# Performance work log

Hardware: AMD Instinct MI355X
Metric: run time of the kernel (lower is better)

## Reference

```python
import jax, jax.numpy as jnp
import numpy as np
from jax import lax

B, L, E, R = 128, 8, 384, 500
HP, HM, HD = 4, 6, 2   # pair-encoder heads, final-mha heads, dynamic-memory heads
MAXLEN = 8
EPS = 1e-5


def _ln(x, g, b):
    m = x.mean(-1, keepdims=True)
    v = ((x - m) ** 2).mean(-1, keepdims=True)
    return (x - m) / jnp.sqrt(v + EPS) * g + b


def _gelu(x):
    return jax.nn.gelu(x, approximate=False)


def _mha(qi, ki, vi, in_w, in_b, out_w, out_b, h):
    # torch nn.MultiheadAttention with packed in_proj ([3E,E]) and out_proj
    Em = qi.shape[-1]
    dh = Em // h
    q = qi @ in_w[:Em].T + in_b[:Em]
    k = ki @ in_w[Em:2 * Em].T + in_b[Em:2 * Em]
    v = vi @ in_w[2 * Em:].T + in_b[2 * Em:]
    def sp(x):
        b_, l_, _ = x.shape
        return x.reshape(b_, l_, h, dh).transpose(0, 2, 1, 3)
    q, k, v = sp(q), sp(k), sp(v)
    a = jax.nn.softmax(jnp.einsum('bhqd,bhkd->bhqk', q, k) / jnp.sqrt(jnp.float32(dh)), axis=-1)
    o = jnp.einsum('bhqk,bhkd->bhqd', a, v).transpose(0, 2, 1, 3).reshape(qi.shape)
    return o @ out_w.T + out_b


def _forward(inputs, emb, rel_pos, qkv_dyn_w, qkv_dyn_b, out_dyn_w, out_dyn_b,
             ln_dyn_g, ln_dyn_b, conv_w, conv_b, tl_in_w, tl_in_b, tl_out_w, tl_out_b,
             tl_ln1_g, tl_ln1_b, tl_ln2_g, tl_ln2_b, tl_ff1_w, tl_ff1_b, tl_ff2_w, tl_ff2_b,
             fc_score_w, fc_score_b, fcq_w, fcq_b, fck_w, fck_b, fcv_w, fcv_b,
             mha_in_w, mha_in_b, mha_out_w, mha_out_b, lnf1_g, lnf1_b, lnf2_g, lnf2_b,
             ff1_w, ff1_b, ff2_w, ff2_b):
    # ---- update_memory: 2-head self-attention over relation embeddings ----
    rel_emb = emb[:R]                                   # [R,E]
    qkv = rel_emb @ qkv_dyn_w.T + qkv_dyn_b             # [R,3E]
    qm, km, vm = jnp.split(qkv, 3, axis=-1)
    dh = E // HD
    def sph(x):
        return x.reshape(R, HD, dh).transpose(1, 0, 2)  # [HD,R,dh]
    qm, km, vm = sph(qm), sph(km), sph(vm)
    am = jax.nn.softmax(jnp.einsum('hqd,hkd->hqk', qm, km) / jnp.sqrt(jnp.float32(dh)), axis=-1)
    om = jnp.einsum('hqk,hkd->hqd', am, vm).transpose(1, 0, 2).reshape(R, E)
    om = om @ out_dyn_w.T + out_dyn_b
    relation_mem = _ln(rel_emb + om, ln_dyn_g, ln_dyn_b)  # [R,E]

    def pair_encode(x):  # x: [N,2,E]  Conv1d(k=3,pad=1) + 2 post-norm transformer layers
        xc = lax.conv_general_dilated(x.transpose(0, 2, 1), conv_w, (1,), [(1, 1)],
                                      dimension_numbers=('NCH', 'OIH', 'NCH'))
        x = (xc + conv_b[None, :, None]).transpose(0, 2, 1)
        for l in range(2):
            a = _mha(x, x, x, tl_in_w[l], tl_in_b[l], tl_out_w[l], tl_out_b[l], HP)
            x = _ln(x + a, tl_ln1_g[l], tl_ln1_b[l])
            f = _gelu(x @ tl_ff1_w[l].T + tl_ff1_b[l]) @ tl_ff2_w[l].T + tl_ff2_b[l]
            x = _ln(x + f, tl_ln2_g[l], tl_ln2_b[l])
        return x

    def fuse(pair):  # pair: [B,1,E] -> memory_attention_fuse
        mem = jnp.concatenate([jnp.broadcast_to(relation_mem[None], (B, R, E)), pair], axis=1)
        q = pair @ fcq_w.T + fcq_b
        k = mem @ fck_w.T + fck_b
        v = mem @ fcv_w.T + fcv_b
        a = _mha(q, k, v, mha_in_w, mha_in_b, mha_out_w, mha_out_b, HM)
        x = _ln(pair + a, lnf1_g, lnf1_b)
        f = _gelu(x @ ff1_w.T + ff1_b) @ ff2_w.T + ff2_b
        return _ln(x + f, lnf2_g, lnf2_b)

    pos = jnp.minimum(jnp.arange(L), MAXLEN - 1)
    seq = emb[inputs] + rel_pos[pos]                    # [B,L,E]

    losses = []
    for _ in range(L - 1):                              # L-1 sequential reduce steps
        Lc = seq.shape[1]
        if Lc <= 2:
            losses.append(jnp.zeros((B, 1), jnp.float32))
            continue
        # all adjacent pairs at once (replaces the per-pair python loop)
        pairs = jnp.stack([seq[:, :-1], seq[:, 1:]], axis=2) + rel_pos[:2]  # [B,Lc-1,2,E]
        hid = pair_encode(pairs.reshape(B * (Lc - 1), 2, E))[:, -1, :].reshape(B, Lc - 1, E)
        sc = jax.nn.sigmoid(hid @ fc_score_w.T + fc_score_b)[..., 0]        # [B,Lc-1]
        idx = jnp.argmax(sc, axis=-1)                                       # [B]
        logp = jax.nn.log_softmax(sc, axis=-1)
        losses.append(-(jnp.exp(logp) * logp).sum(-1, keepdims=True))       # entropy [B,1]
        sel = jnp.take_along_axis(hid, idx[:, None, None], axis=1)          # [B,1,E]
        fused = fuse(sel)                                                   # [B,1,E]
        # scatter fused at idx, delete row idx+1 (compaction)
        updated = jnp.where(jnp.arange(Lc)[None, :, None] == idx[:, None, None], fused, seq)
        gidx = jnp.arange(Lc - 1)[None, :]
        gidx = gidx + (gidx >= (idx + 1)[:, None])
        seq = jnp.take_along_axis(updated, gidx[:, :, None], axis=1)        # [B,Lc-1,E]

    # ---- final memory_attention ----
    Lf = seq.shape[1]  # == 2
    mem = jnp.concatenate([jnp.broadcast_to(relation_mem[None], (B, R, E)), seq], axis=1)
    q = seq @ fcq_w.T + fcq_b
    k = mem @ fck_w.T + fck_b
    a = _mha(q, k, k, mha_in_w, mha_in_b, mha_out_w, mha_out_b, HM)
    x = _ln(seq + a, lnf1_g, lnf1_b)
    f = _gelu(x @ ff1_w.T + ff1_b) @ ff2_w.T + ff2_b
    x = _ln(x + f, lnf2_g, lnf2_b)
    logits = jnp.einsum('ble,bme->blm', x, mem) / jnp.sqrt(jnp.float32(E))
    gate = jnp.ones((R + Lf,), jnp.float32)             # gate_mask buffer is all ones
    logits = logits * gate                              # [B,Lf,R+Lf]
    logp2 = jax.nn.log_softmax(logits, axis=-1)
    ent = -(jnp.exp(logp2) * logp2).sum(-1)             # [B,Lf]
    loss = jnp.concatenate(losses + [ent], axis=-1)     # [B,L+1]
    pred = logits[:, -1, :]                             # [B,R+Lf]
    return pred, loss


def setup_inputs():
    key = jax.random.key(0)
    ctr = [0]
    def nk():
        ctr[0] += 1
        return jax.random.fold_in(key, ctr[0])
    def W(*s):
        return jax.random.normal(nk(), s, jnp.float32) * 0.02
    def Z(*s):
        return jnp.zeros(s, jnp.float32)
    def O(*s):
        return jnp.ones(s, jnp.float32)
    d = {}
    d['inputs'] = jax.random.randint(nk(), (B, L), 0, R)
    d['emb'] = W(R + 1, E).at[R].set(0.0)  # padding_idx row zero
    d['rel_pos'] = W(MAXLEN, E)
    d['qkv_dyn_w'] = W(3 * E, E); d['qkv_dyn_b'] = Z(3 * E)
    d['out_dyn_w'] = W(E, E); d['out_dyn_b'] = Z(E)
    d['ln_dyn_g'] = O(E); d['ln_dyn_b'] = Z(E)
    d['conv_w'] = W(E, E, 3); d['conv_b'] = Z(E)
    d['tl_in_w'] = W(2, 3 * E, E); d['tl_in_b'] = Z(2, 3 * E)
    d['tl_out_w'] = W(2, E, E); d['tl_out_b'] = Z(2, E)
    d['tl_ln1_g'] = O(2, E); d['tl_ln1_b'] = Z(2, E)
    d['tl_ln2_g'] = O(2, E); d['tl_ln2_b'] = Z(2, E)
    d['tl_ff1_w'] = W(2, 4 * E, E); d['tl_ff1_b'] = Z(2, 4 * E)
    d['tl_ff2_w'] = W(2, E, 4 * E); d['tl_ff2_b'] = Z(2, E)
    d['fc_score_w'] = W(1, E); d['fc_score_b'] = Z(1)
    d['fcq_w'] = W(E, E); d['fcq_b'] = Z(E)
    d['fck_w'] = W(E, E); d['fck_b'] = Z(E)
    d['fcv_w'] = W(E, E); d['fcv_b'] = Z(E)
    d['mha_in_w'] = W(3 * E, E); d['mha_in_b'] = Z(3 * E)
    d['mha_out_w'] = W(E, E); d['mha_out_b'] = Z(E)
    d['lnf1_g'] = O(E); d['lnf1_b'] = Z(E)
    d['lnf2_g'] = O(E); d['lnf2_b'] = Z(E)
    d['ff1_w'] = W(4 * E, E); d['ff1_b'] = Z(4 * E)
    d['ff2_w'] = W(E, 4 * E); d['ff2_b'] = Z(E)
    return d


def reference(inputs, emb, rel_pos, qkv_dyn_w, qkv_dyn_b, out_dyn_w, out_dyn_b,
              ln_dyn_g, ln_dyn_b, conv_w, conv_b, tl_in_w, tl_in_b, tl_out_w, tl_out_b,
              tl_ln1_g, tl_ln1_b, tl_ln2_g, tl_ln2_b, tl_ff1_w, tl_ff1_b, tl_ff2_w, tl_ff2_b,
              fc_score_w, fc_score_b, fcq_w, fcq_b, fck_w, fck_b, fcv_w, fcv_b,
              mha_in_w, mha_in_b, mha_out_w, mha_out_b, lnf1_g, lnf1_b, lnf2_g, lnf2_b,
              ff1_w, ff1_b, ff2_w, ff2_b):
    return _forward(inputs, emb, rel_pos, qkv_dyn_w, qkv_dyn_b, out_dyn_w, out_dyn_b,
                    ln_dyn_g, ln_dyn_b, conv_w, conv_b, tl_in_w, tl_in_b, tl_out_w, tl_out_b,
                    tl_ln1_g, tl_ln1_b, tl_ln2_g, tl_ln2_b, tl_ff1_w, tl_ff1_b, tl_ff2_w, tl_ff2_b,
                    fc_score_w, fc_score_b, fcq_w, fcq_b, fck_w, fck_b, fcv_w, fcv_b,
                    mha_in_w, mha_in_b, mha_out_w, mha_out_b, lnf1_g, lnf1_b, lnf2_g, lnf2_b,
                    ff1_w, ff1_b, ff2_w, ff2_b)
```

## Files before the change

kernel.cpp:

```cpp
#include <hip/hip_runtime.h>

#define CDIV(a,b) (((a)+(b)-1)/(b))

typedef __bf16 bf16x8 __attribute__((ext_vector_type(8)));
typedef float  f32x4  __attribute__((ext_vector_type(4)));
#define MFMA16(a,b,c) __builtin_amdgcn_mfma_f32_16x16x32_bf16(a,b,c,0,0,0)

__device__ __forceinline__ float waveSum(float v){
#pragma unroll
  for(int o=32;o;o>>=1) v += __shfl_xor(v,o);
  return v;
}
__device__ __forceinline__ float waveMax(float v){
#pragma unroll
  for(int o=32;o;o>>=1) v = fmaxf(v,__shfl_xor(v,o));
  return v;
}

__device__ __forceinline__ unsigned short f2bf(float f){
  unsigned u = __float_as_uint(f);
  u += 0x7FFFu + ((u>>16)&1u);
  return (unsigned short)(u>>16);
}
__device__ __forceinline__ float bf2f(unsigned short h){
  return __uint_as_float(((unsigned)h)<<16);
}
__device__ __forceinline__ void pack8(const float4& x, const float4& y,
                                      uint4& hi, uint4& lo){
  float v[8] = {x.x,x.y,x.z,x.w,y.x,y.y,y.z,y.w};
  unsigned short h[8], l[8];
#pragma unroll
  for(int i=0;i<8;i++){
    h[i] = f2bf(v[i]);
    l[i] = f2bf(v[i] - bf2f(h[i]));
  }
  hi = make_uint4((unsigned)h[0]|((unsigned)h[1]<<16), (unsigned)h[2]|((unsigned)h[3]<<16),
                  (unsigned)h[4]|((unsigned)h[5]<<16), (unsigned)h[6]|((unsigned)h[7]<<16));
  lo = make_uint4((unsigned)l[0]|((unsigned)l[1]<<16), (unsigned)l[2]|((unsigned)l[3]<<16),
                  (unsigned)l[4]|((unsigned)l[5]<<16), (unsigned)l[6]|((unsigned)l[7]<<16));
}

__device__ __forceinline__ bf16x8 ldsfrag(const unsigned short* base, int row, int kb){
  int off = (row<<7) + (kb<<1);
  off ^= (row&7)<<4;
  return *reinterpret_cast<const bf16x8*>(reinterpret_cast<const char*>(base) + off);
}

template<int ACT>
__global__ __launch_bounds__(256)
void gemm3(const float* __restrict__ A, int lda,
           const float* __restrict__ W, int ldw,
           float* __restrict__ C, int ldc,
           const float* __restrict__ bias, int M, int N, int K, float scale)
{
  __shared__ unsigned short AsH[64*64];
  __shared__ unsigned short AsL[64*64];
  __shared__ unsigned short WsH[64*64];
  __shared__ unsigned short WsL[64*64];
  const int tid  = threadIdx.x;
  const int bm   = blockIdx.x*64, bn = blockIdx.y*64;
  const int lane = tid & 63, wid = tid >> 6;
  const int wm   = (wid&1)*32, wn = (wid>>1)*32;
  const int r0   = tid>>3;
  const int kq   = (tid&7)*8;

  float4 gA[2][2], gW[2][2];
  auto loadG = [&](int k0){
#pragma unroll
    for(int i=0;i<2;i++){
      int r = r0 + i*32;
      if(bm+r < M){
        const float* pa = A + (size_t)(bm+r)*lda + k0 + kq;
        gA[i][0] = *reinterpret_cast<const float4*>(pa);
        gA[i][1] = *reinterpret_cast<const float4*>(pa+4);
      } else {
        gA[i][0] = make_float4(0.f,0.f,0.f,0.f);
        gA[i][1] = make_float4(0.f,0.f,0.f,0.f);
      }
      const float* pw = W + (size_t)(bn+r)*ldw + k0 + kq;
      gW[i][0] = *reinterpret_cast<const float4*>(pw);
      gW[i][1] = *reinterpret_cast<const float4*>(pw+4);
    }
  };
  auto writeL = [&](){
#pragma unroll
    for(int i=0;i<2;i++){
      int r = r0 + i*32;
      int off = (r<<7) + (tid&7)*16;
      off ^= (r&7)<<4;
// ... 91 lines not shown
      } else {
        gA[i][0] = make_float4(0.f,0.f,0.f,0.f);
        gA[i][1] = make_float4(0.f,0.f,0.f,0.f);
      }
      const float* pw = W + (size_t)(bn+r)*ldw + k0 + kq;
      gW[i][0] = *reinterpret_cast<const float4*>(pw);
      gW[i][1] = *reinterpret_cast<const float4*>(pw+4);
    }
  };
  auto writeL = [&](){
#pragma unroll
    for(int i=0;i<2;i++){
      int r = r0 + i*32;
      int off = (r<<7) + (tid&7)*16;
      off ^= (r&7)<<4;
      uint4 hi, lo;
      pack8(gA[i][0], gA[i][1], hi, lo);
      *reinterpret_cast<uint4*>(reinterpret_cast<char*>(AsH) + off) = hi;
      *reinterpret_cast<uint4*>(reinterpret_cast<char*>(AsL) + off) = lo;
      pack8(gW[i][0], gW[i][1], hi, lo);
      *reinterpret_cast<uint4*>(reinterpret_cast<char*>(WsH) + off) = hi;
      *reinterpret_cast<uint4*>(reinterpret_cast<char*>(WsL) + off) = lo;
    }
  };

  f32x4 acc[2][2];
#pragma unroll
  for(int mi=0;mi<2;mi++)
#pragma unroll
    for(int ni=0;ni<2;ni++) acc[mi][ni] = f32x4{0.f,0.f,0.f,0.f};

  loadG(0);
  for(int k0=0; k0<K; k0+=64){
    __syncthreads();
    writeL();
    __syncthreads();
    if(k0+64 < K) loadG(k0+64);
    const int lk = (lane>>4)*8;
    const int lc = lane&15;
#pragma unroll
    for(int kk=0; kk<2; kk++){
      int kb = kk*32 + lk;
      bf16x8 aH[2], aL[2], bH[2], bL[2];
#pragma unroll
      for(int m=0;m<2;m++){
        aH[m] = ldsfrag(AsH, wm + lc + m*16, kb);
        aL[m] = ldsfrag(AsL, wm + lc + m*16, kb);
        bH[m] = ldsfrag(WsH, wn + lc + m*16, kb);
        bL[m] = ldsfrag(WsL, wn + lc + m*16, kb);
      }
#pragma unroll
      for(int mi=0;mi<2;mi++)
#pragma unroll
        for(int ni=0;ni<2;ni++){
          acc[mi][ni] = MFMA16(aH[mi], bH[ni], acc[mi][ni]);
          acc[mi][ni] = MFMA16(aH[mi], bL[ni], acc[mi][ni]);
          acc[mi][ni] = MFMA16(aL[mi], bH[ni], acc[mi][ni]);
        }
    }
  }

  const int lr = lane>>4, lc = lane&15;
#pragma unroll
  for(int mi=0;mi<2;mi++)
#pragma unroll
    for(int ni=0;ni<2;ni++)
#pragma unroll
      for(int r=0;r<4;r++){
        int row = bm + wm + mi*16 + lr*4 + r;
        if(row>=M) continue;
        int col = bn + wn + ni*16 + lc;
        C[(size_t)row*ldc+col] = acc[mi][ni][r]*scale;
      }
}

template<int ACT>
__global__ __launch_bounds__(256)
void gemm3s(const float* __restrict__ A, int lda,
            const unsigned short* __restrict__ WH,
            const unsigned short* __restrict__ WL, int ldw,
            float* __restrict__ C, int ldc,
            const float* __restrict__ bias, int M, int N, int K)
{
  __shared__ unsigned short AsH[64*64];
  __shared__ unsigned short AsL[64*64];
  __shared__ unsigned short WsH[64*64];
  __shared__ unsigned short WsL[64*64];
  const int tid  = threadIdx.x;
  const int bm   = blockIdx.x*64, bn = blockIdx.y*64;
  const int lane = tid & 63, wid = tid >> 6;
  const int wm   = (wid&1)*32, wn = (wid>>1)*32;
  const int r0   = tid>>3;
  const int kq   = (tid&7)*8;

  float4 gA[2][2]; uint4 gWH[2], gWL[2];
  auto loadG = [&](int k0){
#pragma unroll
    for(int i=0;i<2;i++){
      int r = r0 + i*32;
      if(bm+r < M){
        const float* pa = A + (size_t)(bm+r)*lda + k0 + kq;
        gA[i][0] = *reinterpret_cast<const float4*>(pa);
        gA[i][1] = *reinterpret_cast<const float4*>(pa+4);
      } else {
        gA[i][0] = make_float4(0.f,0.f,0.f,0.f);
        gA[i][1] = make_float4(0.f,0.f,0.f,0.f);
      }
      gWH[i] = *reinterpret_cast<const uint4*>(WH + (size_t)(bn+r)*ldw + k0 + kq);
      gWL[i] = *reinterpret_cast<const uint4*>(WL + (size_t)(bn+r)*ldw + k0 + kq);
    }
  };
  auto writeL = [&](){
#pragma unroll
    for(int i=0;i<2;i++){
      int r = r0 + i*32;
      int off = (r<<7) + (tid&7)*16;
      off ^= (r&7)<<4;
      uint4 hi, lo;
      pack8(gA[i][0], gA[i][1], hi, lo);
      *reinterpret_cast<uint4*>(reinterpret_cast<char*>(AsH) + off) = hi;
      *reinterpret_cast<uint4*>(reinterpret_cast<char*>(AsL) + off) = lo;
      *reinterpret_cast<uint4*>(reinterpret_cast<char*>(WsH) + off) = gWH[i];
      *reinterpret_cast<uint4*>(reinterpret_cast<char*>(WsL) + off) = gWL[i];
    }
  };

  f32x4 acc[2][2];
#pragma unroll
  for(int mi=0;mi<2;mi++)
#pragma unroll
    for(int ni=0;ni<2;ni++) acc[mi][ni] = f32x4{0.f,0.f,0.f,0.f};

  loadG(0);
  for(int k0=0; k0<K; k0+=64){
    __syncthreads();
    writeL();
    __syncthreads();
    if(k0+64 < K) loadG(k0+64);
    const int lk = (lane>>4)*8;
    const int lc = lane&15;
#pragma unroll
    for(int kk=0; kk<2; kk++){
      int kb = kk*32 + lk;
      bf16x8 aH[2], aL[2], bH[2], bL[2];
#pragma unroll
      for(int m=0;m<2;m++){
        aH[m] = ldsfrag(AsH, wm + lc + m*16, kb);
        aL[m] = ldsfrag(AsL, wm + lc + m*16, kb);
        bH[m] = ldsfrag(WsH, wn + lc + m*16, kb);
        bL[m] = ldsfrag(WsL, wn + lc + m*16, kb);
      }
#pragma unroll
      for(int mi=0;mi<2;mi++)
#pragma unroll
        for(int ni=0;ni<2;ni++){
          acc[mi][ni] = MFMA16(aH[mi], bH[ni], acc[mi][ni]);
          acc[mi][ni] = MFMA16(aH[mi], bL[ni], acc[mi][ni]);
          acc[mi][ni] = MFMA16(aL[mi], bH[ni], acc[mi][ni]);
        }
    }
  }

  const int lr = lane>>4, lc = lane&15;
#pragma unroll
  for(int mi=0;mi<2;mi++)
#pragma unroll
    for(int ni=0;ni<2;ni++)
#pragma unroll
      for(int r=0;r<4;r++){
        int row = bm + wm + mi*16 + lr*4 + r;
        if(row>=M) continue;
        int col = bn + wn + ni*16 + lc;
        float v = acc[mi][ni][r] + (bias ? bias[col] : 0.f);
        if(ACT==1) v = 0.5f*v*(1.f+erff(v*0.70710678118654752f));
        C[(size_t)row*ldc+col] = v;
      }
}

__global__ __launch_bounds__(256)
void gemm3bk(const float* __restrict__ A0, int lda, int sAz,
             const unsigned short* __restrict__ WH0,
             const unsigned short* __restrict__ WL0, int ldw, int sWz,
             float* __restrict__ Cp, int M, int N, int KLEN, int KS)
{
  __shared__ unsigned short AsH[64*64];
  __shared__ unsigned short AsL[64*64];
  __shared__ unsigned short WsH[64*64];
  __shared__ unsigned short WsL[64*64];
  const int z  = blockIdx.z;
  const int bz = z / KS, ks = z - bz*KS;
  const float* A = A0 + (size_t)bz*sAz;
  const unsigned short* WH = WH0 + (size_t)bz*sWz;
  const unsigned short* WL = WL0 + (size_t)bz*sWz;
  const int kbeg = ks*KLEN, kend = kbeg + KLEN;
  const int tid  = threadIdx.x;
  const int bm   = blockIdx.x*64, bn = blockIdx.y*64;
  const int lane = tid & 63, wid = tid >> 6;
  const int wm   = (wid&1)*32, wn = (wid>>1)*32;
  const int r0   = tid>>3;
  const int kq   = (tid&7)*8;

  float4 gA[2][2]; uint4 gWH[2], gWL[2];
  auto loadG = [&](int k0){
#pragma unroll
    for(int i=0;i<2;i++){
      int r = r0 + i*32;
      if(bm+r < M){
        const float* pa = A + (size_t)(bm+r)*lda + k0 + kq;
        gA[i][0] = *reinterpret_cast<const float4*>(pa);
        gA[i][1] = *reinterpret_cast<const float4*>(pa+4);
      } else {
        gA[i][0] = make_float4(0.f,0.f,0.f,0.f);
        gA[i][1] = make_float4(0.f,0.f,0.f,0.f);
      }
      gWH[i] = *reinterpret_cast<const uint4*>(WH + (size_t)(bn+r)*ldw + k0 + kq);
      gWL[i] = *reinterpret_cast<const uint4*>(WL + (size_t)(bn+r)*ldw + k0 + kq);
    }
  };
  auto writeL = [&](){
#pragma unroll
    for(int i=0;i<2;i++){
      int r = r0 + i*32;
      int off = (r<<7) + (tid&7)*16;
      off ^= (r&7)<<4;
      uint4 hi, lo;
      pack8(gA[i][0], gA[i][1], hi, lo);
      *reinterpret_cast<uint4*>(reinterpret_cast<char*>(AsH) + off) = hi;
      *reinterpret_cast<uint4*>(reinterpret_cast<char*>(AsL) + off) = lo;
      *reinterpret_cast<uint4*>(reinterpret_cast<char*>(WsH) + off) = gWH[i];
      *reinterpret_cast<uint4*>(reinterpret_cast<char*>(WsL) + off) = gWL[i];
    }
  };

  f32x4 acc[2][2];
#pragma unroll
  for(int mi=0;mi<2;mi++)
#pragma unroll
    for(int ni=0;ni<2;ni++) acc[mi][ni] = f32x4{0.f,0.f,0.f,0.f};

  loadG(kbeg);
  for(int k0=kbeg; k0<kend; k0+=64){
    __syncthreads();
    writeL();
    __syncthreads();
    if(k0+64 < kend) loadG(k0+64);
    const int lk = (lane>>4)*8;
    const int lc = lane&15;
#pragma unroll
    for(int kk=0; kk<2; kk++){
      int kb = kk*32 + lk;
      bf16x8 aH[2], aL[2], bH[2], bL[2];
#pragma unroll
      for(int m=0;m<2;m++){
        aH[m] = ldsfrag(AsH, wm + lc + m*16, kb);
        aL[m] = ldsfrag(AsL, wm + lc + m*16, kb);
        bH[m] = ldsfrag(WsH, wn + lc + m*16, kb);
        bL[m] = ldsfrag(WsL, wn + lc + m*16, kb);
      }
#pragma unroll
      for(int mi=0;mi<2;mi++)
#pragma unroll
        for(int ni=0;ni<2;ni++){
          acc[mi][ni] = MFMA16(aH[mi], bH[ni], acc[mi][ni]);
          acc[mi][ni] = MFMA16(aH[mi], bL[ni], acc[mi][ni]);
          acc[mi][ni] = MFMA16(aL[mi], bH[ni], acc[mi][ni]);
        }
    }
  }

  float* Cpz = Cp + (size_t)z*M*N;
  const int lr = lane>>4, lc = lane&15;
#pragma unroll
  for(int mi=0;mi<2;mi++)
#pragma unroll
    for(int ni=0;ni<2;ni++)
#pragma unroll
      for(int r=0;r<4;r++){
        int row = bm + wm + mi*16 + lr*4 + r;
        if(row>=M) continue;
        int col = bn + wn + ni*16 + lc;
        Cpz[(size_t)row*N+col] = acc[mi][ni][r];
      }
}

template<int ACT>
__global__ __launch_bounds__(256)
void reduce_k(const float* __restrict__ Cp, float* __restrict__ C,
              const float* __restrict__ bias, int MN, int N, int ldc,
              int sCz, int KS, int NB, float scale)
{
  int gid = blockIdx.x*256+threadIdx.x;
  if(gid >= NB*MN) return;
  int b = gid / MN, e = gid - b*MN;
  int m = e / N, n = e - m*N;
  const float* p = Cp + (size_t)b*KS*MN + e;
  float s = 0.f;
  for(int k=0;k<KS;k++) s += p[(size_t)k*MN];
  s = s*scale + (bias ? bias[n] : 0.f);
  if(ACT==1) s = 0.5f*s*(1.f+erff(s*0.70710678118654752f));
  C[(size_t)b*sCz + (size_t)m*ldc + n] = s;
}

__global__ __launch_bounds__(128)
void reduce_ln(const float* __restrict__ Pp, const float* __restrict__ X,
               float* __restrict__ O, const float* __restrict__ g,
               const float* __restrict__ be, const float* __restrict__ bias,
               int M, int KS)
{
  int row = blockIdx.x;
  if(row>=M) return;
  int tid = threadIdx.x;
  const float* x = X + (size_t)row*384;
  float* o = O + (size_t)row*384;
  float v[3]; float s=0.f;
#pragma unroll
  for(int i=0;i<3;i++){
    int c = tid + i*128;
    float t = bias ? bias[c] : 0.f;
    const float* p = Pp + (size_t)row*384 + c;
    for(int k=0;k<KS;k++) t += p[(size_t)k*M*384];
    v[i] = x[c] + t; s += v[i];
  }
  s = waveSum(s);
  __shared__ float p1[2];
  if((tid&63)==0) p1[tid>>6]=s;
  __syncthreads();
  float mean = (p1[0]+p1[1])*(1.f/384.f);
  float vs=0.f;
#pragma unroll
  for(int i=0;i<3;i++){ float d=v[i]-mean; vs += d*d; }
  vs = waveSum(vs);
  __shared__ float p2[2];
  if((tid&63)==0) p2[tid>>6]=vs;
  __syncthreads();
  float rstd = rsqrtf((p2[0]+p2[1])*(1.f/384.f) + 1e-5f);
#pragma unroll
  for(int i=0;i<3;i++){ int c = tid + i*128; o[c] = (v[i]-mean)*rstd*g[c] + be[c]; }
}

__global__ __launch_bounds__(256)
void gemm_nn(const float* __restrict__ A, int lda,
             const float* __restrict__ Bm, int ldb,
             float* __restrict__ C, int ldc,
             int M, int N, int K, float scale)
{
  __shared__ float As[16][68];
  __shared__ float Bs[16][68];
  const int bm = blockIdx.x*64, bn = blockIdx.y*64;
  const int tid = threadIdx.x;
  const int lr = tid>>2;
// ... 69 lines not shown
__global__ __launch_bounds__(256)
void softmax_rows(float* __restrict__ X, int ld, int cols)
{
  float* x = X + (size_t)blockIdx.x*ld;
  int tid = threadIdx.x;
  float m = -1e30f;
  for(int c=tid;c<cols;c+=256) m = fmaxf(m, x[c]);
  m = waveMax(m);
  __shared__ float sm[4];
  if((tid&63)==0) sm[tid>>6]=m;
  __syncthreads();
  m = fmaxf(fmaxf(sm[0],sm[1]),fmaxf(sm[2],sm[3]));
  float s=0.f;
  for(int c=tid;c<cols;c+=256){ float e = expf(x[c]-m); x[c]=e; s+=e; }
  s = waveSum(s);
  __shared__ float ss[4];
  if((tid&63)==0) ss[tid>>6]=s;
  __syncthreads();
  s = ss[0]+ss[1]+ss[2]+ss[3];
  float inv = 1.f/s;
  for(int c=tid;c<cols;c+=256) x[c]*=inv;
  for(int c=cols+tid;c<ld;c+=256) x[c]=0.f;
}

__global__ void prep_conv(const float* __restrict__ cw, const float* __restrict__ cb,
                          float* __restrict__ Wc, float* __restrict__ cb768){
  int gid = blockIdx.x*256+threadIdx.x;
  if(gid >= 384*384) return;
  int i = gid % 384, o = gid / 384;
  const float* w = cw + (size_t)gid*3;
  Wc[(size_t)o*768 + i]            = w[1];
  Wc[(size_t)o*768 + 384 + i]      = w[2];
  Wc[(size_t)(384+o)*768 + i]      = w[0];
  Wc[(size_t)(384+o)*768 + 384 + i]= w[1];
  if(gid < 768) cb768[gid] = cb[gid % 384];
}

__global__ void vt_k(const float* __restrict__ qkv, float* __restrict__ VT){
  int gid = blockIdx.x*256+threadIdx.x;
  if(gid >= 2*192*512) return;
  int k = gid & 511; int n = (gid>>9) % 192; int h = gid / 98304;
  VT[gid] = (k<500) ? qkv[(size_t)k*1152 + 768 + h*192 + n] : 0.f;
}

__global__ void prep_attn(const float* __restrict__ K1, const float* __restrict__ Vf,
                          const float* __restrict__ Vl, float* __restrict__ Kp,
                          float* __restrict__ VTf, float* __restrict__ VTl){
  int gid = blockIdx.x*256+threadIdx.x;
  if(gid < 196608){
    int j = gid / 384;
    Kp[gid] = (j<500) ? K1[gid] : 0.f;
    return;
  }
  int g2 = gid - 196608;
  const float* V; float* VT;
  if(g2 < 196608){ V = Vf; VT = VTf; }
  else { g2 -= 196608; if(g2 >= 196608) return; V = Vl; VT = VTl; }
  int j = g2 & 511; int d = (g2>>9) & 63; int h = g2 >> 15;
  VT[g2] = (j<500) ? V[(size_t)j*384 + h*64 + d] : 0.f;
}

__global__ void compose_bias(const float* __restrict__ inw, const float* __restrict__ inb,
                             const float* __restrict__ qb, const float* __restrict__ kb,
                             const float* __restrict__ vb, float* __restrict__ cb){
  int gid = blockIdx.x*256+threadIdx.x;
  if(gid>=1536) return;
  int seg = gid/384, i = gid%384;
  const float* wrow; const float* bsrc; float b2;
  if(seg==0){ wrow=inw + (size_t)i*384;       bsrc=qb; b2=inb[i]; }
  else if(seg==1){ wrow=inw + (size_t)(384+i)*384; bsrc=kb; b2=inb[384+i]; }
  else if(seg==2){ wrow=inw + (size_t)(768+i)*384; bsrc=vb; b2=inb[768+i]; }
  else          { wrow=inw + (size_t)(768+i)*384; bsrc=kb; b2=inb[768+i]; }
  float s=0.f;
  for(int t=0;t<384;t++) s = fmaf(wrow[t], bsrc[t], s);
  cb[gid] = s + b2;
}

#define NSEG 18
struct SplitArgs {
  const float* src[NSEG];
  unsigned short* dh[NSEG];
  unsigned short* dl[NSEG];
  int start[NSEG+1];
};
__global__ void split_all(SplitArgs a){
  int gid = blockIdx.x*256+threadIdx.x;
  if(gid >= a.start[NSEG]) return;
  int s=0;
  while(s<NSEG-1 && gid >= a.start[s+1]) s++;
  int off = gid - a.start[s];
  float v = a.src[s][off];
  unsigned short h = f2bf(v);
  a.dh[s][off] = h;
  a.dl[s][off] = f2bf(v - bf2f(h));
}

__global__ void seq_init(const int* __restrict__ inp, const float* __restrict__ emb,
                         const float* __restrict__ rp, float* __restrict__ seq){
  int gid = blockIdx.x*256+threadIdx.x;
  if(gid >= 128*8*384) return;
  int j = gid % 384; int l = (gid/384) & 7; int b = gid / 3072;
  int tok = inp[b*8 + l];
  seq[gid] = emb[(size_t)tok*384 + j] + rp[l*384 + j];
}

__global__ void build_pairs(const float* __restrict__ seq, const float* __restrict__ rp,
                            float* __restrict__ pairs, int N, int P){
  int gid = blockIdx.x*256+threadIdx.x;
  if(gid >= N*768) return;
  int c = gid % 768; int n = gid / 768;
  int t = c / 384; int j = c % 384;
  int i = n % P; int b = n / P;
  pairs[gid] = seq[((size_t)b*8 + i + t)*384 + j] + rp[t*384 + j];
}

__global__ __launch_bounds__(256)
void attn2_one(const float* __restrict__ QKV, float* __restrict__ O, int N){
  int n = blockIdx.x;
  if(n>=N) return;
  int tid = threadIdx.x, lane = tid&63, h = tid>>6;
  __shared__ float pr[4][2][2];
  const float* base = QKV + (size_t)(2*n)*1152;
  const float* q0 = base + h*96;
  const float* q1 = base + 1152 + h*96;
  const float* k0 = base + 384 + h*96;
  const float* k1 = base + 1152 + 384 + h*96;
  float q0a=q0[lane], q1a=q1[lane], k0a=k0[lane], k1a=k1[lane];
  float q0b=0.f,q1b=0.f,k0b=0.f,k1b=0.f;
  if(lane<32){ q0b=q0[64+lane]; q1b=q1[64+lane]; k0b=k0[64+lane]; k1b=k1[64+lane]; }
  float s00 = waveSum(q0a*k0a + q0b*k0b);
  float s01 = waveSum(q0a*k1a + q0b*k1b);
  float s10 = waveSum(q1a*k0a + q1b*k0b);
  float s11 = waveSum(q1a*k1a + q1b*k1b);
  if(lane==0){
    const float sc = 0.1020620726159658f;
    s00*=sc; s01*=sc; s10*=sc; s11*=sc;
    float m0=fmaxf(s00,s01); float e00=expf(s00-m0), e01=expf(s01-m0); float i0=1.f/(e00+e01);
    float m1=fmaxf(s10,s11); float e10=expf(s10-m1), e11=expf(s11-m1); float i1=1.f/(e10+e11);
    pr[h][0][0]=e00*i0; pr[h][0][1]=e01*i0;
    pr[h][1][0]=e10*i1; pr[h][1][1]=e11*i1;
  }
  __syncthreads();
  const float* v0 = base + 768;
  const float* v1 = base + 1152 + 768;
  float* o = O + (size_t)(2*n)*384;
#pragma unroll
  for(int i=0;i<3;i++){
    int c = tid + i*256;
    int t = c / 384, j = c % 384; int hh = j/96;
    o[(size_t)t*384 + j] = pr[hh][t][0]*v0[j] + pr[hh][t][1]*v1[j];
  }
}

__global__ void extract_hid(const float* __restrict__ xb, float* __restrict__ hid){
  int gid = blockIdx.x*256+threadIdx.x;
  if(gid >= 128*7*384) return;
  int j = gid % 384; int n = gid / 384;
  hid[gid] = xb[((size_t)(2*n+1))*384 + j];
}

__global__ void scatter_hid(const float* __restrict__ xb, const int* __restrict__ idxb,
                            float* __restrict__ hid, int P){
  int gid = blockIdx.x*256+threadIdx.x;
  if(gid >= 256*384) return;
  int j = gid % 384; int r = gid / 384; int b = r>>1; int e = r&1;
  int s = idxb[b]-1+e; s = max(0, min(s, P-1));
  hid[((size_t)b*7 + s)*384 + j] = xb[((size_t)(2*r+1))*384 + j];
}

__global__ __launch_bounds__(256)
void score_select2(const float* __restrict__ hid, const float* __restrict__ w,
                   const float* __restrict__ b0, int P, int* __restrict__ idxb,
                   float* __restrict__ lossSlot, float* __restrict__ sel){
  int b = blockIdx.x;
  int tid = threadIdx.x, lane = tid&63, wv = tid>>6;
  __shared__ float scs[8];
  __shared__ int sidx;
// ... 231 lines not shown
  float* cb     = Aa(1536);
  float* cb768  = Aa(768);
  float* seqA_  = Aa(393216);
  float* seqB_  = Aa(393216);
  float* hidA_  = Aa(344064);
  float* hidB_  = Aa(344064);
  float* fqkv1  = Aa(147456);
  float* gqkv1  = Aa(294912);
  unsigned short* SH = (unsigned short*)Aa(3514368);
  unsigned short* SL = (unsigned short*)Aa(3514368);
  float* Pp     = Aa(2359296);
  float* pairs  = Aa(688128);
  float* xbuf   = Aa(688128);
  float* qkvbuf = Aa(2064384);
  float* obuf   = Aa(688128);
  float* tmpb   = Aa(688128);
  float* ffbuf  = Aa(2752512);
  float* probs2 = Aa(14336);
  int*   idxb   = (int*)Aa(128);
  float* sel    = Aa(49152);
  float* fo     = Aa(49152);
  float* fxf    = Aa(49152);
  float* ffused = Aa(49152);
  float* fffb   = Aa(196608);

  float* sc512   = ffbuf;
  float* Cfuse3f = ffbuf + 600000;
  float* Cvkf    = ffbuf + 1100000;
  float* Wconvf  = ffbuf + 1300000;
  float* VT      = tmpb;
  float* Sbuf = ffbuf;
  float* Ebuf = probs2;
  float* seqf = pairs;
  float* go   = obuf;
  float* gx1  = obuf + 196608;
  float* gx2  = obuf + 294912;
  float* logitsb = qkvbuf;

  float* lossBase = (float*)d_out + 128*502;

  const int o_qkvdyn=0, o_outdyn=442368, o_wconv=589824,
            o_tlin0=1179648, o_tlin1=1622016, o_tlout0=2064384, o_tlout1=2211840,
            o_tlff1_0=2359296, o_tlff1_1=2949120, o_tlff2_0=3538944, o_tlff2_1=4128768,
            o_mhaout=4718592, o_ff1=4866048, o_ff2=5455872, o_cfuse=6045696, o_cvk=6488064,
            o_vtf=6635520, o_vtl=6832128;
  const int split_total = 7028736;

  const float s192 = 0.07216878364870322f;

  gemm3<0><<<dim3(8,18),256,0,stream>>>(emb,384, qkv_dyn_w,384, qkvbuf,1152, qkv_dyn_b, 500,1152,384, 1.f);
  for(int h=0;h<2;h++)
    gemm3<0><<<dim3(8,8),256,0,stream>>>(qkvbuf + h*192,1152, qkvbuf + 384 + h*192,1152,
           sc512 + (size_t)h*256000,512, nullptr, 500,512,192, s192);
  softmax_rows<<<1000,256,0,stream>>>(sc512, 512, 500);
  vt_k<<<CDIV(2*192*512,256),256,0,stream>>>(qkvbuf, VT);
  for(int h=0;h<2;h++)
    gemm3<0><<<dim3(8,3),256,0,stream>>>(sc512 + (size_t)h*256000,512, VT + h*98304,512,
           obuf + h*192,384, nullptr, 500,192,512, 1.f);
  gemm3<0><<<dim3(8,6),256,0,stream>>>(obuf,384, out_dyn_w,384, xbuf,384, out_dyn_b, 500,384,384, 1.f);
  add_ln<<<500,128,0,stream>>>(emb, xbuf, relmem, ln_dyn_g, ln_dyn_b, 500);

  gemm_nn<<<dim3(6,6),256,0,stream>>>(mha_in_w,384,            fcq_w,384, Cfuse3f,384,          384,384,384, 1.f);
  gemm_nn<<<dim3(6,6),256,0,stream>>>(mha_in_w + 384*384,384,  fck_w,384, Cfuse3f + 147456,384, 384,384,384, 1.f);
  gemm_nn<<<dim3(6,6),256,0,stream>>>(mha_in_w + 768*384,384,  fcv_w,384, Cfuse3f + 294912,384, 384,384,384, 1.f);
  gemm_nn<<<dim3(6,6),256,0,stream>>>(mha_in_w + 768*384,384,  fck_w,384, Cvkf,384,             384,384,384, 1.f);
  compose_bias<<<6,256,0,stream>>>(mha_in_w, mha_in_b, fcq_b, fck_b, fcv_b, cb);

  gemm3<0><<<dim3(8,6),256,0,stream>>>(relmem,384, Cfuse3f + 147456,384, K1mem,384, cb+384,  500,384,384, 1.f);
  gemm3<0><<<dim3(8,6),256,0,stream>>>(relmem,384, Cfuse3f + 294912,384, V1f,384,   cb+768,  500,384,384, 1.f);
  gemm3<0><<<dim3(8,6),256,0,stream>>>(relmem,384, Cvkf,384,            V1l,384,   cb+1152, 500,384,384, 1.f);
  prep_attn<<<CDIV(3*196608,256),256,0,stream>>>(K1mem, V1f, V1l, K1padf, VT1f, VT1lf);

  prep_conv<<<CDIV(384*384,256),256,0,stream>>>(conv_w, conv_b, Wconvf, cb768);

  {
    SplitArgs a;
    const float* srcs[NSEG] = { qkv_dyn_w, out_dyn_w, Wconvf, tl_in_w, tl_in_w + 442368,
                                tl_out_w, tl_out_w + 147456, tl_ff1_w, tl_ff1_w + 589824,
                                tl_ff2_w, tl_ff2_w + 589824, mha_out_w, ff1_w, ff2_w,
                                Cfuse3f, Cvkf, VT1f, VT1lf };
    const int offs[NSEG+1] = { o_qkvdyn, o_outdyn, o_wconv, o_tlin0, o_tlin1, o_tlout0, o_tlout1,
                               o_tlff1_0, o_tlff1_1, o_tlff2_0, o_tlff2_1, o_mhaout, o_ff1, o_ff2,
                               o_cfuse, o_cvk, o_vtf, o_vtl, split_total };
    for(int s=0;s<NSEG;s++){
      a.src[s]=srcs[s]; a.dh[s]=SH+offs[s]; a.dl[s]=SL+offs[s]; a.start[s]=offs[s];
    }
    a.start[NSEG]=split_total;
    split_all<<<CDIV(split_total,256),256,0,stream>>>(a);
  }
  seq_init<<<CDIV(128*8*384,256),256,0,stream>>>(inputs, emb, rel_pos, seqA_);

  float* seqCur = seqA_; float* seqNxt = seqB_;
  float* hidCur = hidA_; float* hidNxt = hidB_;

  for(int it=0; it<6; ++it){
    int P = 7 - it;
    if(it == 0){
      int N = 128*7, R2 = 2*N;
      build_pairs<<<CDIV(N*768,256),256,0,stream>>>(seqCur, rel_pos, pairs, N, 7);
      gemm3s<0><<<dim3(N/64,12),256,0,stream>>>(pairs,768, SH+o_wconv,SL+o_wconv,768,
                                                xbuf,768, cb768, N,768,768);
      for(int l=0;l<2;l++){
        int oin  = l? o_tlin1  : o_tlin0;
        int oout = l? o_tlout1 : o_tlout0;
        int of1  = l? o_tlff1_1: o_tlff1_0;
        int of2  = l? o_tlff2_1: o_tlff2_0;
        gemm3s<0><<<dim3(R2/64,18),256,0,stream>>>(xbuf,384, SH+oin,SL+oin,384,
                                                   qkvbuf,1152, tl_in_b + l*1152, R2,1152,384);
        attn2_one<<<N,256,0,stream>>>(qkvbuf, obuf, N);
        gemm3s<0><<<dim3(R2/64,6),256,0,stream>>>(obuf,384, SH+oout,SL+oout,384,
                                                  tmpb,384, tl_out_b + l*384, R2,384,384);
        add_ln<<<R2,128,0,stream>>>(xbuf, tmpb, xbuf, tl_ln1_g + l*384, tl_ln1_b + l*384, R2);
        gemm3s<1><<<dim3(R2/64,24),256,0,stream>>>(xbuf,384, SH+of1,SL+of1,384,
                                                   ffbuf,1536, tl_ff1_b + l*1536, R2,1536,384);
        gemm3s<0><<<dim3(R2/64,6),256,0,stream>>>(ffbuf,1536, SH+of2,SL+of2,1536,
                                                  tmpb,384, tl_ff2_b + l*384, R2,384,1536);
        add_ln<<<R2,128,0,stream>>>(xbuf, tmpb, xbuf, tl_ln2_g + l*384, tl_ln2_b + l*384, R2);
      }
      extract_hid<<<CDIV(128*7*384,256),256,0,stream>>>(xbuf, hidCur);
    } else {
      const int N2 = 256, R2 = 512;
      gemm3bk<<<dim3(4,12,12),256,0,stream>>>(pairs,768,0, SH+o_wconv,SL+o_wconv,768,0,
                                              Pp, N2,768,64,12);
      reduce_k<0><<<CDIV(N2*768,256),256,0,stream>>>(Pp, xbuf, cb768, N2*768,768,768,0,12,1, 1.f);
      for(int l=0;l<2;l++){
        int oin  = l? o_tlin1  : o_tlin0;
        int oout = l? o_tlout1 : o_tlout0;
        int of1  = l? o_tlff1_1: o_tlff1_0;
        int of2  = l? o_tlff2_1: o_tlff2_0;
        gemm3s<0><<<dim3(R2/64,18),256,0,stream>>>(xbuf,384, SH+oin,SL+oin,384,
                                                   qkvbuf,1152, tl_in_b + l*1152, R2,1152,384);
        attn2_one<<<N2,256,0,stream>>>(qkvbuf, obuf, N2);
        gemm3bk<<<dim3(R2/64,6,6),256,0,stream>>>(obuf,384,0, SH+oout,SL+oout,384,0,
                                                  Pp, R2,384,64,6);
        reduce_ln<<<R2,128,0,stream>>>(Pp, xbuf, xbuf, tl_ln1_g + l*384, tl_ln1_b + l*384,
                                       tl_out_b + l*384, R2, 6);
        gemm3s<1><<<dim3(R2/64,24),256,0,stream>>>(xbuf,384, SH+of1,SL+of1,384,
                                                   ffbuf,1536, tl_ff1_b + l*1536, R2,1536,384);
        gemm3bk<<<dim3(R2/64,6,8),256,0,stream>>>(ffbuf,1536,0, SH+of2,SL+of2,1536,0,
                                                  Pp, R2,384,192,8);
        reduce_ln<<<R2,128,0,stream>>>(Pp, xbuf, xbuf, tl_ln2_g + l*384, tl_ln2_b + l*384,
                                       tl_ff2_b + l*384, R2, 8);
      }
      scatter_hid<<<CDIV(256*384,256),256,0,stream>>>(xbuf, idxb, hidCur, P);
    }
    score_select2<<<128,256,0,stream>>>(hidCur, fc_score_w, fc_score_b, P, idxb, lossBase + it, sel);
    gemm3bk<<<dim3(2,18,6),256,0,stream>>>(sel,384,0, SH+o_cfuse,SL+o_cfuse,384,0,
                                           Pp, 128,1152,64,6);
    reduce_k<0><<<CDIV(128*1152,256),256,0,stream>>>(Pp, fqkv1, cb, 128*1152,1152,1152,0,6,1, 1.f);
    gemm3z<<<dim3(2,8,6),256,0,stream>>>(fqkv1,1152,64, K1padf,384,64,
                                         Sbuf,512,128*512, 128,512,64, 0.125f);
    softmax_ext2<1><<<768,256,0,stream>>>(Sbuf, fqkv1, Ebuf, 128);
    gemm3bk<<<dim3(2,1,48),256,0,stream>>>(Sbuf,512,65536, SH+o_vtf,SL+o_vtf,512,32768,
                                           Pp, 128,64,64,8);
    pv_epi2<1><<<CDIV(128*384,256),256,0,stream>>>(Pp, Ebuf, fqkv1, fo, 128);
    gemm3bk<<<dim3(2,6,6),256,0,stream>>>(fo,384,0, SH+o_mhaout,SL+o_mhaout,384,0,
                                          Pp, 128,384,64,6);
    reduce_ln<<<128,128,0,stream>>>(Pp, sel, fxf, lnf1_g, lnf1_b, mha_out_b, 128, 6);
    gemm3bk<<<dim3(2,24,6),256,0,stream>>>(fxf,384,0, SH+o_ff1,SL+o_ff1,384,0,
                                           Pp, 128,1536,64,6);
    reduce_k<1><<<CDIV(128*1536,256),256,0,stream>>>(Pp, fffb, ff1_b, 128*1536,1536,1536,0,6,1, 1.f);
    gemm3bk<<<dim3(2,6,24),256,0,stream>>>(fffb,1536,0, SH+o_ff2,SL+o_ff2,1536,0,
                                           Pp, 128,384,64,24);
    reduce_ln<<<128,128,0,stream>>>(Pp, fxf, ffused, lnf2_g, lnf2_b, ff2_b, 128, 24);
    {
      int last = (it==5) ? 1 : 0;
      int total = 128*P*384 + (last ? 0 : (128*(P-1)*384 + 256*768));
      merge_all<<<CDIV(total,256),256,0,stream>>>(seqCur, ffused, hidCur, rel_pos, idxb,
// ... 33 lines not shown
```

Baseline: 2.006 ms.

## Pre-tile split weights and stream them into double-buffered LDS via async loads

The weight split kernel now writes the hi/lo bf16 weights in a 64x64-tiled, XOR-swizzled layout, so each weight tile is contiguous. The gemm3s and gemm3bk kernels load those tiles straight into LDS with global_load_lds, double-buffered, instead of staging them through registers. The aim is to cut register pressure and VALU/LDS-write work on the weight path and to overlap the next tile's weight fetch with the current MFMA compute. It relies on every weight passed to these kernels using the tiled layout and on K being a multiple of 64. It also doubles the weight LDS footprint, which may lower occupancy.

Result: faster. 1.716 ms (-14.5%).

```diff
diff --git a/kernel.cpp b/kernel.cpp
--- a/kernel.cpp
+++ b/kernel.cpp
@@ -5,6 +5,12 @@
 typedef __bf16 bf16x8 __attribute__((ext_vector_type(8)));
 typedef float  f32x4  __attribute__((ext_vector_type(4)));
 #define MFMA16(a,b,c) __builtin_amdgcn_mfma_f32_16x16x32_bf16(a,b,c,0,0,0)
+
+__device__ __forceinline__ void ldst16(const unsigned short* g, unsigned short* l){
+  __builtin_amdgcn_global_load_lds(
+      (const __attribute__((address_space(1))) unsigned int*)g,
+      (__attribute__((address_space(3))) unsigned int*)l, 16, 0, 0);
+}
 
 __device__ __forceinline__ float waveSum(float v){
 #pragma unroll
@@ -262,19 +268,23 @@
             float* __restrict__ C, int ldc,
             const float* __restrict__ bias, int M, int N, int K)
 {
-  __shared__ unsigned short AsH[64*64];
-  __shared__ unsigned short AsL[64*64];
-  __shared__ unsigned short WsH[64*64];
-  __shared__ unsigned short WsL[64*64];
+  __shared__ unsigned short AsH[4096];
+  __shared__ unsigned short AsL[4096];
+  __shared__ unsigned short WsH0[4096], WsL0[4096];
+  __shared__ unsigned short WsH1[4096], WsL1[4096];
   const int tid  = threadIdx.x;
   const int bm   = blockIdx.x*64, bn = blockIdx.y*64;
   const int lane = tid & 63, wid = tid >> 6;
   const int wm   = (wid&1)*32, wn = (wid>>1)*32;
   const int r0   = tid>>3;
   const int kq   = (tid&7)*8;
-
-  float4 gA[2][2]; uint4 gWH[2], gWL[2];
-  auto loadG = [&](int k0){
+  const int KT   = ldw >> 6;
+  const unsigned short* WHt = WH + (size_t)(bn>>6)*KT*4096;
+  const unsigned short* WLt = WL + (size_t)(bn>>6)*KT*4096;
+  const int wbase = wid*1024;
+
+  float4 gA[2][2];
+  auto loadGA = [&](int k0){
 #pragma unroll
     for(int i=0;i<2;i++){
       int r = r0 + i*32;
@@ -286,11 +296,9 @@
         gA[i][0] = make_float4(0.f,0.f,0.f,0.f);
         gA[i][1] = make_float4(0.f,0.f,0.f,0.f);
       }
-      gWH[i] = *reinterpret_cast<const uint4*>(WH + (size_t)(bn+r)*ldw + k0 + kq);
-      gWL[i] = *reinterpret_cast<const uint4*>(WL + (size_t)(bn+r)*ldw + k0 + kq);
     }
   };
-  auto writeL = [&](){
+  auto writeLA = [&](){
 #pragma unroll
     for(int i=0;i<2;i++){
       int r = r0 + i*32;
@@ -300,10 +308,16 @@
       pack8(gA[i][0], gA[i][1], hi, lo);
       *reinterpret_cast<uint4*>(reinterpret_cast<char*>(AsH) + off) = hi;
       *reinterpret_cast<uint4*>(reinterpret_cast<char*>(AsL) + off) = lo;
-      *reinterpret_cast<uint4*>(reinterpret_cast<char*>(WsH) + off) = gWH[i];
-      *reinterpret_cast<uint4*>(reinterpret_cast<char*>(WsL) + off) = gWL[i];
     }
   };
+  auto asyncW = [&](int kt, unsigned short* dH, unsigned short* dL){
+    const unsigned short* gh = WHt + (size_t)kt*4096 + wbase + lane*8;
+    const unsigned short* gl = WLt + (size_t)kt*4096 + wbase + lane*8;
+    ldst16(gh,       dH + wbase);
+    ldst16(gh + 512, dH + wbase + 512);
+    ldst16(gl,       dL + wbase);
+    ldst16(gl + 512, dL + wbase + 512);
+  };
 
   f32x4 acc[2][2];
 #pragma unroll
@@ -311,12 +325,7 @@
 #pragma unroll
     for(int ni=0;ni<2;ni++) acc[mi][ni] = f32x4{0.f,0.f,0.f,0.f};
 
-  loadG(0);
-  for(int k0=0; k0<K; k0+=64){
-    __syncthreads();
-    writeL();
-    __syncthreads();
-    if(k0+64 < K) loadG(k0+64);
+  auto compute = [&](const unsigned short* Wh, const unsigned short* Wl){
     const int lk = (lane>>4)*8;
     const int lc = lane&15;
 #pragma unroll
@@ -327,8 +336,8 @@
       for(int m=0;m<2;m++){
         aH[m] = ldsfrag(AsH, wm + lc + m*16, kb);
         aL[m] = ldsfrag(AsL, wm + lc + m*16, kb);
-        bH[m] = ldsfrag(WsH, wn + lc + m*16, kb);
-        bL[m] = ldsfrag(WsL, wn + lc + m*16, kb);
+        bH[m] = ldsfrag(Wh, wn + lc + m*16, kb);
+        bL[m] = ldsfrag(Wl, wn + lc + m*16, kb);
       }
 #pragma unroll
       for(int mi=0;mi<2;mi++)
@@ -339,6 +348,26 @@
           acc[mi][ni] = MFMA16(aL[mi], bH[ni], acc[mi][ni]);
         }
     }
+  };
+
+  asyncW(0, WsH0, WsL0);
+  loadGA(0);
+  int k0 = 0, kt = 0;
+  while(true){
+    __syncthreads();
+    writeLA();
+    __syncthreads();
+    if(k0+64 < K){ asyncW(kt+1, WsH1, WsL1); loadGA(k0+64); }
+    compute(WsH0, WsL0);
+    k0 += 64; kt++;
+    if(k0 >= K) break;
+    __syncthreads();
+    writeLA();
+    __syncthreads();
+    if(k0+64 < K){ asyncW(kt+1, WsH0, WsL0); loadGA(k0+64); }
+    compute(WsH1, WsL1);
+    k0 += 64; kt++;
+    if(k0 >= K) break;
   }
 
   const int lr = lane>>4, lc = lane&15;
@@ -363,10 +392,10 @@
              const unsigned short* __restrict__ WL0, int ldw, int sWz,
              float* __restrict__ Cp, int M, int N, int KLEN, int KS)
 {
-  __shared__ unsigned short AsH[64*64];
-  __shared__ unsigned short AsL[64*64];
-  __shared__ unsigned short WsH[64*64];
-  __shared__ unsigned short WsL[64*64];
+  __shared__ unsigned short AsH[4096];
+  __shared__ unsigned short AsL[4096];
+  __shared__ unsigned short WsH0[4096], WsL0[4096];
+  __shared__ unsigned short WsH1[4096], WsL1[4096];
   const int z  = blockIdx.z;
   const int bz = z / KS, ks = z - bz*KS;
   const float* A = A0 + (size_t)bz*sAz;
@@ -379,9 +408,13 @@
   const int wm   = (wid&1)*32, wn = (wid>>1)*32;
   const int r0   = tid>>3;
   const int kq   = (tid&7)*8;
-
-  float4 gA[2][2]; uint4 gWH[2], gWL[2];
-  auto loadG = [&](int k0){
+  const int KT   = ldw >> 6;
+  const unsigned short* WHt = WH + (size_t)(bn>>6)*KT*4096;
+  const unsigned short* WLt = WL + (size_t)(bn>>6)*KT*4096;
+  const int wbase = wid*1024;
+
+  float4 gA[2][2];
+  auto loadGA = [&](int k0){
 #pragma unroll
     for(int i=0;i<2;i++){
       int r = r0 + i*32;
@@ -393,11 +426,9 @@
         gA[i][0] = make_float4(0.f,0.f,0.f,0.f);
         gA[i][1] = make_float4(0.f,0.f,0.f,0.f);
       }
-      gWH[i] = *reinterpret_cast<const uint4*>(WH + (size_t)(bn+r)*ldw + k0 + kq);
-      gWL[i] = *reinterpret_cast<const uint4*>(WL + (size_t)(bn+r)*ldw + k0 + kq);
     }
   };
-  auto writeL = [&](){
+  auto writeLA = [&](){
 #pragma unroll
     for(int i=0;i<2;i++){
       int r = r0 + i*32;
@@ -407,10 +438,16 @@
       pack8(gA[i][0], gA[i][1], hi, lo);
       *reinterpret_cast<uint4*>(reinterpret_cast<char*>(AsH) + off) = hi;
       *reinterpret_cast<uint4*>(reinterpret_cast<char*>(AsL) + off) = lo;
-      *reinterpret_cast<uint4*>(reinterpret_cast<char*>(WsH) + off) = gWH[i];
-      *reinterpret_cast<uint4*>(reinterpret_cast<char*>(WsL) + off) = gWL[i];
     }
   };
+  auto asyncW = [&](int kt, unsigned short* dH, unsigned short* dL){
+    const unsigned short* gh = WHt + (size_t)kt*4096 + wbase + lane*8;
+    const unsigned short* gl = WLt + (size_t)kt*4096 + wbase + lane*8;
+    ldst16(gh,       dH + wbase);
+    ldst16(gh + 512, dH + wbase + 512);
+    ldst16(gl,       dL + wbase);
+    ldst16(gl + 512, dL + wbase + 512);
+  };
 
   f32x4 acc[2][2];
 #pragma unroll
@@ -418,12 +455,7 @@
 #pragma unroll
     for(int ni=0;ni<2;ni++) acc[mi][ni] = f32x4{0.f,0.f,0.f,0.f};
 
-  loadG(kbeg);
-  for(int k0=kbeg; k0<kend; k0+=64){
-    __syncthreads();
-    writeL();
-    __syncthreads();
-    if(k0+64 < kend) loadG(k0+64);
+  auto compute = [&](const unsigned short* Wh, const unsigned short* Wl){
     const int lk = (lane>>4)*8;
     const int lc = lane&15;
 #pragma unroll
@@ -434,8 +466,8 @@
       for(int m=0;m<2;m++){
         aH[m] = ldsfrag(AsH, wm + lc + m*16, kb);
         aL[m] = ldsfrag(AsL, wm + lc + m*16, kb);
-        bH[m] = ldsfrag(WsH, wn + lc + m*16, kb);
-        bL[m] = ldsfrag(WsL, wn + lc + m*16, kb);
+        bH[m] = ldsfrag(Wh, wn + lc + m*16, kb);
+        bL[m] = ldsfrag(Wl, wn + lc + m*16, kb);
       }
 #pragma unroll
       for(int mi=0;mi<2;mi++)
@@ -446,6 +478,26 @@
           acc[mi][ni] = MFMA16(aL[mi], bH[ni], acc[mi][ni]);
         }
     }
+  };
+
+  asyncW(kbeg>>6, WsH0, WsL0);
+  loadGA(kbeg);
+  int k0 = kbeg, kt = kbeg>>6;
+  while(true){
+    __syncthreads();
+    writeLA();
+    __syncthreads();
+    if(k0+64 < kend){ asyncW(kt+1, WsH1, WsL1); loadGA(k0+64); }
+    compute(WsH0, WsL0);
+    k0 += 64; kt++;
+    if(k0 >= kend) break;
+    __syncthreads();
+    writeLA();
+    __syncthreads();
+    if(k0+64 < kend){ asyncW(kt+1, WsH0, WsL0); loadGA(k0+64); }
+    compute(WsH1, WsL1);
+    k0 += 64; kt++;
+    if(k0 >= kend) break;
   }
 
   float* Cpz = Cp + (size_t)z*M*N;
@@ -681,6 +733,7 @@
   unsigned short* dh[NSEG];
   unsigned short* dl[NSEG];
   int start[NSEG+1];
+  int ld[NSEG];
 };
 __global__ void split_all(SplitArgs a){
   int gid = blockIdx.x*256+threadIdx.x;
@@ -688,10 +741,13 @@
   int s=0;
   while(s<NSEG-1 && gid >= a.start[s+1]) s++;
   int off = gid - a.start[s];
+  int K = a.ld[s];
+  int r = off / K, c = off - r*K;
+  int dst = ((r>>6)*(K>>6) + (c>>6))*4096 + ((r&63)<<6) + ((c&63) ^ ((r&7)<<3));
   float v = a.src[s][off];
   unsigned short h = f2bf(v);
-  a.dh[s][off] = h;
-  a.dl[s][off] = f2bf(v - bf2f(h));
+  a.dh[s][dst] = h;
+  a.dl[s][dst] = f2bf(v - bf2f(h));
 }
 
 __global__ void seq_init(const int* __restrict__ inp, const float* __restrict__ emb,
@@ -1089,8 +1145,11 @@
     const int offs[NSEG+1] = { o_qkvdyn, o_outdyn, o_wconv, o_tlin0, o_tlin1, o_tlout0, o_tlout1,
                                o_tlff1_0, o_tlff1_1, o_tlff2_0, o_tlff2_1, o_mhaout, o_ff1, o_ff2,
                                o_cfuse, o_cvk, o_vtf, o_vtl, split_total };
+    const int lds[NSEG] = { 384, 384, 768, 384, 384, 384, 384, 384, 384,
+                            1536, 1536, 384, 384, 1536, 384, 384, 512, 512 };
     for(int s=0;s<NSEG;s++){
       a.src[s]=srcs[s]; a.dh[s]=SH+offs[s]; a.dl[s]=SL+offs[s]; a.start[s]=offs[s];
+      a.ld[s]=lds[s];
     }
     a.start[NSEG]=split_total;
     split_all<<<CDIV(split_total,256),256,0,stream>>>(a);
```
